# Optimization experiments

Measured on AMD Instinct MI355X. Metric: run time of the kernel, lower is better.

Reference implementation:

```python
import jax, jax.numpy as jnp
import numpy as np

N = 100000   # nodes
E = 3200000  # edges (avg degree 32)
D0, D1, D2, OUT = 128, 64, 64, 10


def setup_inputs() -> dict:
    key = jax.random.key(0)
    ks = jax.random.split(key, 6)
    x = jax.random.normal(ks[0], (N, D0), jnp.float32)
    edge_index = jax.random.randint(ks[1], (2, E), 0, N, jnp.int32)
    Wa1 = jax.random.normal(ks[2], (D0, D1), jnp.float32) / np.sqrt(D0).astype(np.float32)
    ba1 = jnp.zeros((D1,), jnp.float32)
    Wa2 = jax.random.normal(ks[3], (D1, D2), jnp.float32) / np.sqrt(D1).astype(np.float32)
    ba2 = jnp.zeros((D2,), jnp.float32)
    Wl = jax.random.normal(ks[4], (D2 * D2, OUT), jnp.float32) / np.sqrt(D2 * D2).astype(np.float32)
    bl = jnp.zeros((OUT,), jnp.float32)
    return {"x": x, "edge_index": edge_index, "Wa1": Wa1, "ba1": ba1,
            "Wa2": Wa2, "ba2": ba2, "Wl": Wl, "bl": bl}


def _gcn(x, W, b, src, dst, norm):
    # GCNConv: D^{-1/2} (A+I) D^{-1/2} X W + b  (self-loops already in src/dst)
    h = x @ W                                  # [N, Dout]
    m = h[src] * norm[:, None]                 # gather + scale  [E+N, Dout]
    return jax.ops.segment_sum(m, dst, num_segments=N) + b


def reference(x, edge_index, Wa1, ba1, Wa2, ba2, Wl, bl):
    loops = jnp.arange(N, dtype=edge_index.dtype)
    src = jnp.concatenate([edge_index[0], loops])
    dst = jnp.concatenate([edge_index[1], loops])
    deg = jax.ops.segment_sum(jnp.ones_like(src, jnp.float32), dst, num_segments=N)
    dinv = jax.lax.rsqrt(deg)                  # deg >= 1 thanks to self-loops
    norm = dinv[src] * dinv[dst]

    a1 = _gcn(x, Wa1, ba1, src, dst, norm)
    a2 = _gcn(a1, Wa2, ba2, src, dst, norm)
    # Original reuses gcn_a1/gcn_a2 for the x-path, so x_2 == a_2 exactly.
    x2 = a2
    h = a2.T @ x2                              # [D2, D2] attention-style readout
    o = h.reshape(1, -1) @ Wl + bl             # [1, OUT]
    return jax.nn.softmax(o, axis=-1)
```

## Files before the change

kernel.cpp:

```cpp
#include <hip/hip_runtime.h>


#define CHUNK 4096
#define BSH   8

__global__ __launch_bounds__(256) void hist_pass(const int* __restrict__ dst,
                                                 int* __restrict__ ghist,
                                                 int E, int nblk, int nbuck) {
    __shared__ int lcnt[512];
    const int blk = blockIdx.x;
    for (int i = threadIdx.x; i < nbuck; i += 256) lcnt[i] = 0;
    __syncthreads();
    const int base = blk * CHUNK;
    const int end  = min(base + CHUNK, E);
    for (int e = base + threadIdx.x; e < end; e += 256) {
        int d = __builtin_nontemporal_load(&dst[e]);
        atomicAdd(&lcnt[d >> BSH], 1);
    }
    __syncthreads();
    for (int b = threadIdx.x; b < nbuck; b += 256)
        ghist[(size_t)b * nblk + blk] = lcnt[b];
}

__global__ __launch_bounds__(256) void scan_blocks(int* __restrict__ ghist,
                                                   int* __restrict__ btot, int nblk) {
    __shared__ int sh[256];
    int* g = ghist + (size_t)blockIdx.x * nblk;
    const int tid = threadIdx.x;
    int carry = 0;
    for (int base = 0; base < nblk; base += 256) {
        int i = base + tid;
        int v = (i < nblk) ? g[i] : 0;
        sh[tid] = v;
        __syncthreads();
        for (int off = 1; off < 256; off <<= 1) {
            int t = (tid >= off) ? sh[tid - off] : 0;
            __syncthreads();
            sh[tid] += t;
            __syncthreads();
        }
        if (i < nblk) g[i] = carry + sh[tid] - v;
        int tot = sh[255];
        __syncthreads();
        carry += tot;
    }
    if (tid == 0) btot[blockIdx.x] = carry;
}

__global__ void scan_bstart(const int* __restrict__ btot, int* __restrict__ bstart, int nb) {
    __shared__ int sh[512];
    const int tid = threadIdx.x;
    int v = (tid < nb) ? btot[tid] : 0;
    sh[tid] = v;
    __syncthreads();
    for (int off = 1; off < 512; off <<= 1) {
        int t = (tid >= off) ? sh[tid - off] : 0;
        __syncthreads();
        sh[tid] += t;
        __syncthreads();
    }
    if (tid < nb) bstart[tid] = sh[tid] - v;
}

__global__ __launch_bounds__(256) void place_pass(const int* __restrict__ src,
                                                  const int* __restrict__ dst,
                                                  const int* __restrict__ ghist,
                                                  const int* __restrict__ bstart,
                                                  uint2* __restrict__ bedges,
                                                  int E, int nblk, int nbuck) {
    __shared__ int off[512];
    const int blk = blockIdx.x;
    for (int b = threadIdx.x; b < nbuck; b += 256)
        off[b] = bstart[b] + ghist[(size_t)b * nblk + blk];
    __syncthreads();
    const int base = blk * CHUNK;
    const int end  = min(base + CHUNK, E);
    for (int e = base + threadIdx.x; e < end; e += 256) {
        int d = __builtin_nontemporal_load(&dst[e]);
        int s = __builtin_nontemporal_load(&src[e]);
        int pos = atomicAdd(&off[d >> BSH], 1);
        bedges[pos] = make_uint2((unsigned)s, (unsigned)(d & 255));
    }
}

__global__ __launch_bounds__(256) void bucket_csr(const uint2* __restrict__ bedges,
                                                  const int* __restrict__ btot,
                                                  const int* __restrict__ bstart,
                                                  float* __restrict__ dinv,
                                                  int* __restrict__ rowptr,
                                                  int* __restrict__ rowend,
                                                  int* __restrict__ ssorted, int N) {
    __shared__ int lcnt[256];
    __shared__ int sc[256];
    __shared__ int lcur[256];
    const int b   = blockIdx.x;
    const int tid = threadIdx.x;
    const int cnt  = btot[b];
    const int base = bstart[b];
    lcnt[tid] = 0;
    __syncthreads();
    for (int i = tid; i < cnt; i += 256)
        atomicAdd(&lcnt[(int)bedges[base + i].y], 1);
    __syncthreads();
    int c = lcnt[tid];
    sc[tid] = c;
    __syncthreads();
    for (int off = 1; off < 256; off <<= 1) {
        int t = (tid >= off) ? sc[tid - off] : 0;
        __syncthreads();
        sc[tid] += t;
        __syncthreads();
    }
    const int excl = sc[tid] - c;
    const int n = (b << BSH) + tid;
    if (n < N) {
        dinv[n]   = rsqrtf((float)c + 1.0f);
        rowptr[n] = base + excl;
        rowend[n] = base + excl + c;
    }
    lcur[tid] = excl;
    __syncthreads();
    for (int i = tid; i < cnt; i += 256) {
        uint2 e = bedges[base + i];
        int pos = atomicAdd(&lcur[(int)e.y], 1);
        ssorted[base + pos] = (int)e.x;
    }
}

template <int K>
__global__ __launch_bounds__(256) void gemm_tiled(const float* __restrict__ A,
                                                  const float* __restrict__ W,
                                                  const float* __restrict__ dinv,
                                                  float* __restrict__ H, int N) {
    constexpr int KC = 32;
    __shared__ float xs[64][KC + 4];
    __shared__ float ws[KC][64];
    const int tid  = threadIdx.x;
    const int tx   = tid & 15;
    const int ty   = tid >> 4;
    const int base = blockIdx.x * 64;

    float acc[4][4] = {{0.f}};

    for (int kc = 0; kc < K; kc += KC) {
        for (int idx = tid; idx < 512; idx += 256) {
            int node = idx >> 3, k4 = idx & 7;
            int n = base + node;
            float4 v = make_float4(0.f, 0.f, 0.f, 0.f);
            if (n < N) v = *(const float4*)&A[(long long)n * K + kc + k4 * 4];
            *(float4*)&xs[node][k4 * 4] = v;
        }
        for (int idx = tid; idx < 512; idx += 256) {
            int k = idx >> 4, c4 = idx & 15;
            *(float4*)&ws[k][c4 * 4] = *(const float4*)&W[(long long)(kc + k) * 64 + c4 * 4];
        }
        __syncthreads();

#pragma unroll
        for (int k = 0; k < KC; k += 4) {
            float4 xv[4], wv[4];
#pragma unroll
            for (int i = 0; i < 4; ++i) xv[i] = *(const float4*)&xs[ty * 4 + i][k];
#pragma unroll
            for (int j = 0; j < 4; ++j) wv[j] = *(const float4*)&ws[k + j][tx * 4];
#pragma unroll
            for (int i = 0; i < 4; ++i) {
                float xi[4] = {xv[i].x, xv[i].y, xv[i].z, xv[i].w};
#pragma unroll
                for (int j = 0; j < 4; ++j) {
                    acc[i][0] += xi[j] * wv[j].x;
                    acc[i][1] += xi[j] * wv[j].y;
                    acc[i][2] += xi[j] * wv[j].z;
                    acc[i][3] += xi[j] * wv[j].w;
                }
            }
        }
        __syncthreads();
    }

#pragma unroll
    for (int i = 0; i < 4; ++i) {
        int n = base + ty * 4 + i;
        if (n < N) {
            float d = dinv[n];
            float4 r = make_float4(d * acc[i][0], d * acc[i][1], d * acc[i][2], d * acc[i][3]);
            *(float4*)&H[(long long)n * 64 + tx * 4] = r;
        }
    }
}

__global__ void agg_csr(const int* __restrict__ rowptr, const int* __restrict__ endptr,
                        const int* __restrict__ ssorted, const float* __restrict__ dinv,
                        const float* __restrict__ H, const float* __restrict__ bias,
                        float* __restrict__ out, int N) {
    const int wid  = (int)(((long long)blockIdx.x * blockDim.x + threadIdx.x) >> 6);
    if (wid >= N) return;
    const int lane = threadIdx.x & 63;
    const int g    = lane >> 4;
    const int fl   = lane & 15;
    const float4* __restrict__ Hv = (const float4*)H;

    const int   n   = wid;
    const int   beg = rowptr[n];
    const int   end = endptr[n];

    float4 acc = make_float4(0.f, 0.f, 0.f, 0.f);
    for (int e = beg + g; e < end; e += 4) {
        int    s  = ssorted[e];
        float4 hv = Hv[(long long)s * 16 + fl];
        acc.x += hv.x; acc.y += hv.y; acc.z += hv.z; acc.w += hv.w;
    }
    acc.x += __shfl_xor(acc.x, 16); acc.y += __shfl_xor(acc.y, 16);
    acc.z += __shfl_xor(acc.z, 16); acc.w += __shfl_xor(acc.w, 16);
    acc.x += __shfl_xor(acc.x, 32); acc.y += __shfl_xor(acc.y, 32);
    acc.z += __shfl_xor(acc.z, 32); acc.w += __shfl_xor(acc.w, 32);

    if (g == 0) {
        float4 selfv = Hv[(long long)n * 16 + fl];
        float4 bv    = ((const float4*)bias)[fl];
        float  dn    = dinv[n];
        float4 res;
        res.x = bv.x + dn * (selfv.x + acc.x);
        res.y = bv.y + dn * (selfv.y + acc.y);
        res.z = bv.z + dn * (selfv.z + acc.z);
        res.w = bv.w + dn * (selfv.w + acc.w);
        ((float4*)out)[(long long)n * 16 + fl] = res;
    }
}

__global__ void outer_reduce(const float* __restrict__ A2, float* __restrict__ h64, int N) {
    __shared__ float rows[8][64];
    const int tid = threadIdx.x;
    const int col = tid & 63;
    const int rg  = tid >> 6;
    float acc[16];
#pragma unroll
    for (int i = 0; i < 16; ++i) acc[i] = 0.f;

    int npb   = (N + gridDim.x - 1) / gridDim.x;
    int start = blockIdx.x * npb;
    int end   = min(start + npb, N);
    for (int nb = start; nb < end; nb += 8) {
        int cnt = min(8, end - nb);
        __syncthreads();
        for (int idx = tid; idx < cnt * 64; idx += 256)
            rows[idx >> 6][idx & 63] = A2[(long long)(nb + (idx >> 6)) * 64 + (idx & 63)];
        __syncthreads();
        for (int r = 0; r < cnt; ++r) {
            float vc = rows[r][col];
#pragma unroll
            for (int i = 0; i < 16; ++i)
                acc[i] += rows[r][rg * 16 + i] * vc;
        }
    }
#pragma unroll
    for (int i = 0; i < 16; ++i)
        atomicAdd(&h64[(rg * 16 + i) * 64 + col], acc[i]);
}

__global__ void final_kernel(const float* __restrict__ h64, const float* __restrict__ Wl,
                             const float* __restrict__ bl, float* __restrict__ out) {
    __shared__ float red[256];
    __shared__ float o[10];
    const int tid = threadIdx.x;
    float acc[10];
#pragma unroll
    for (int k = 0; k < 10; ++k) acc[k] = 0.f;
    for (int i = tid; i < 4096; i += 256) {
        float v = h64[i];
#pragma unroll
        for (int k = 0; k < 10; ++k) acc[k] += v * Wl[i * 10 + k];
    }
    for (int k = 0; k < 10; ++k) {
        red[tid] = acc[k];
        __syncthreads();
        for (int s = 128; s > 0; s >>= 1) {
            if (tid < s) red[tid] += red[tid + s];
            __syncthreads();
        }
        if (tid == 0) o[k] = red[0] + bl[k];
        __syncthreads();
    }
    if (tid == 0) {
        float m = o[0];
        for (int k = 1; k < 10; ++k) m = fmaxf(m, o[k]);
        float s = 0.f, e[10];
        for (int k = 0; k < 10; ++k) { e[k] = expf(o[k] - m); s += e[k]; }
        for (int k = 0; k < 10; ++k) out[k] = e[k] / s;
    }
}

extern "C" void kernel_launch(void* const* d_in, const int* in_sizes, int n_in,
                              void* d_out, int out_size, void* d_ws, size_t ws_size,
                              hipStream_t stream) {
    const float* x   = (const float*)d_in[0];
    const int*   ei  = (const int*)d_in[1];
    const float* Wa1 = (const float*)d_in[2];
    const float* ba1 = (const float*)d_in[3];
    const float* Wa2 = (const float*)d_in[4];
    const float* ba2 = (const float*)d_in[5];
    const float* Wl  = (const float*)d_in[6];
    const float* bl  = (const float*)d_in[7];
    float* out = (float*)d_out;

    const int N = in_sizes[0] / 128;
    const int E = in_sizes[1] / 2;
    const int* src = ei;
    const int* dst = ei + E;

    const int nblk  = (E + CHUNK - 1) / CHUNK;
    const int nbuck = (N + 255) >> BSH;

    char* wsb = (char*)d_ws;
    float* bufH   = (float*)wsb;
    float* bufA   = bufH + (size_t)N * 64;
    uint2* bedges = (uint2*)wsb;
    int*   ghist  = (int*)(wsb + (size_t)E * 8);
    int*   btot   = ghist + (size_t)nbuck * nblk;
    int*   bstart = btot + 512;
    char*  tail   = wsb + (size_t)N * 128 * 4;
    float* dinv   = (float*)tail;               tail += (size_t)N * 4;
    float* h64    = (float*)tail;               tail += 4096 * 4;
    int*   rowptr = (int*)tail;                 tail += (size_t)N * 4;
    int*   rowend = (int*)tail;                 tail += (size_t)N * 4;
    int*   ssorted= (int*)tail;                 tail += (size_t)E * 4;

    hist_pass<<<nblk, 256, 0, stream>>>(dst, ghist, E, nblk, nbuck);
    scan_blocks<<<nbuck, 256, 0, stream>>>(ghist, btot, nblk);
    scan_bstart<<<1, 512, 0, stream>>>(btot, bstart, nbuck);
    place_pass<<<nblk, 256, 0, stream>>>(src, dst, ghist, bstart, bedges, E, nblk, nbuck);
    bucket_csr<<<nbuck, 256, 0, stream>>>(bedges, btot, bstart, dinv, rowptr, rowend, ssorted, N);

    gemm_tiled<128><<<(N + 63) / 64, 256, 0, stream>>>(x, Wa1, dinv, bufH, N);
    agg_csr<<<(N + 3) / 4, 256, 0, stream>>>(rowptr, rowend, ssorted, dinv, bufH, ba1, bufA, N);

    gemm_tiled<64><<<(N + 63) / 64, 256, 0, stream>>>(bufA, Wa2, dinv, bufH, N);
    agg_csr<<<(N + 3) / 4, 256, 0, stream>>>(rowptr, rowend, ssorted, dinv, bufH, ba2, bufA, N);

    hipMemsetAsync(h64, 0, 4096 * sizeof(float), stream);
    outer_reduce<<<512, 256, 0, stream>>>(bufA, h64, N);
    final_kernel<<<1, 256, 0, stream>>>(h64, Wl, bl, out);
}
```

Baseline: 547.9 us.

## Store hidden features feature-planar and aggregate in sixteen cache-sized passes

The GEMM now writes H as 16 planes of float4, one per group of four features, instead of node-major rows. Aggregation runs one pass per plane, with one wavefront per node gathering a single float4 per edge, so each pass gathers from a table of about 1.6 MB that should stay in L2. The cost is that the sorted-source list is read 16 times, and with an average degree near 32 about half the lanes in each wavefront sit idle. The outer-product reduction now writes per-block partials followed by a reduction kernel instead of using atomics, and the final kernel gives each output one wavefront with a shuffle reduction.

```diff
diff --git a/kernel.cpp b/kernel.cpp
--- a/kernel.cpp
+++ b/kernel.cpp
@@ -127,7 +127,7 @@
     }
 }
 
-template <int K>
+template <int K, bool PM_IN>
 __global__ __launch_bounds__(256) void gemm_tiled(const float* __restrict__ A,
                                                   const float* __restrict__ W,
                                                   const float* __restrict__ dinv,
@@ -139,16 +139,28 @@
     const int tx   = tid & 15;
     const int ty   = tid >> 4;
     const int base = blockIdx.x * 64;
+    const float4* __restrict__ Av4 = (const float4*)A;
+    float4* __restrict__ Hp4 = (float4*)H;
 
     float acc[4][4] = {{0.f}};
 
     for (int kc = 0; kc < K; kc += KC) {
-        for (int idx = tid; idx < 512; idx += 256) {
-            int node = idx >> 3, k4 = idx & 7;
-            int n = base + node;
-            float4 v = make_float4(0.f, 0.f, 0.f, 0.f);
-            if (n < N) v = *(const float4*)&A[(long long)n * K + kc + k4 * 4];
-            *(float4*)&xs[node][k4 * 4] = v;
+        if (PM_IN) {
+            for (int idx = tid; idx < 512; idx += 256) {
+                int node = idx & 63, k4l = idx >> 6;
+                int n = base + node;
+                float4 v = make_float4(0.f, 0.f, 0.f, 0.f);
+                if (n < N) v = Av4[(size_t)(kc / 4 + k4l) * N + n];
+                *(float4*)&xs[node][k4l * 4] = v;
+            }
+        } else {
+            for (int idx = tid; idx < 512; idx += 256) {
+                int node = idx >> 3, k4 = idx & 7;
+                int n = base + node;
+                float4 v = make_float4(0.f, 0.f, 0.f, 0.f);
+                if (n < N) v = *(const float4*)&A[(long long)n * K + kc + k4 * 4];
+                *(float4*)&xs[node][k4 * 4] = v;
+            }
         }
         for (int idx = tid; idx < 512; idx += 256) {
             int k = idx >> 4, c4 = idx & 15;
@@ -184,55 +196,61 @@
         if (n < N) {
             float d = dinv[n];
             float4 r = make_float4(d * acc[i][0], d * acc[i][1], d * acc[i][2], d * acc[i][3]);
-            *(float4*)&H[(long long)n * 64 + tx * 4] = r;
-        }
-    }
-}
-
-__global__ void agg_csr(const int* __restrict__ rowptr, const int* __restrict__ endptr,
-                        const int* __restrict__ ssorted, const float* __restrict__ dinv,
-                        const float* __restrict__ H, const float* __restrict__ bias,
-                        float* __restrict__ out, int N) {
-    const int wid  = (int)(((long long)blockIdx.x * blockDim.x + threadIdx.x) >> 6);
-    if (wid >= N) return;
+            Hp4[(size_t)tx * N + n] = r;
+        }
+    }
+}
+
+#define NPASS 16
+__global__ __launch_bounds__(256) void agg_pass(const int* __restrict__ rowptr,
+                                                const int* __restrict__ rowend,
+                                                const int* __restrict__ ssorted,
+                                                const float* __restrict__ dinv,
+                                                const float* __restrict__ H,
+                                                const float* __restrict__ bias,
+                                                float* __restrict__ out,
+                                                int N, int npb) {
+    const int pass = blockIdx.x / npb;
+    const int nb   = blockIdx.x % npb;
+    const int n    = nb * 4 + (threadIdx.x >> 6);
+    if (n >= N) return;
     const int lane = threadIdx.x & 63;
-    const int g    = lane >> 4;
-    const int fl   = lane & 15;
-    const float4* __restrict__ Hv = (const float4*)H;
-
-    const int   n   = wid;
-    const int   beg = rowptr[n];
-    const int   end = endptr[n];
-
-    float4 acc = make_float4(0.f, 0.f, 0.f, 0.f);
-    for (int e = beg + g; e < end; e += 4) {
-        int    s  = ssorted[e];
-        float4 hv = Hv[(long long)s * 16 + fl];
-        acc.x += hv.x; acc.y += hv.y; acc.z += hv.z; acc.w += hv.w;
-    }
-    acc.x += __shfl_xor(acc.x, 16); acc.y += __shfl_xor(acc.y, 16);
-    acc.z += __shfl_xor(acc.z, 16); acc.w += __shfl_xor(acc.w, 16);
-    acc.x += __shfl_xor(acc.x, 32); acc.y += __shfl_xor(acc.y, 32);
-    acc.z += __shfl_xor(acc.z, 32); acc.w += __shfl_xor(acc.w, 32);
-
-    if (g == 0) {
-        float4 selfv = Hv[(long long)n * 16 + fl];
-        float4 bv    = ((const float4*)bias)[fl];
-        float  dn    = dinv[n];
-        float4 res;
-        res.x = bv.x + dn * (selfv.x + acc.x);
-        res.y = bv.y + dn * (selfv.y + acc.y);
-        res.z = bv.z + dn * (selfv.z + acc.z);
-        res.w = bv.w + dn * (selfv.w + acc.w);
-        ((float4*)out)[(long long)n * 16 + fl] = res;
-    }
-}
-
-__global__ void outer_reduce(const float* __restrict__ A2, float* __restrict__ h64, int N) {
+    const float4* __restrict__ Hs = (const float4*)H + (size_t)pass * N;
+
+    const int beg = rowptr[n];
+    const int end = rowend[n];
+
+    float4 a = make_float4(0.f, 0.f, 0.f, 0.f);
+    for (int e = beg + lane; e < end; e += 64) {
+        int    s = __builtin_nontemporal_load(&ssorted[e]);
+        float4 h = Hs[s];
+        a.x += h.x; a.y += h.y; a.z += h.z; a.w += h.w;
+    }
+#pragma unroll
+    for (int m = 1; m < 64; m <<= 1) {
+        a.x += __shfl_xor(a.x, m); a.y += __shfl_xor(a.y, m);
+        a.z += __shfl_xor(a.z, m); a.w += __shfl_xor(a.w, m);
+    }
+    if (lane == 0) {
+        float  dn = dinv[n];
+        float4 sv = Hs[n];
+        float4 bv = ((const float4*)bias)[pass];
+        float4 r;
+        r.x = bv.x + dn * (sv.x + a.x);
+        r.y = bv.y + dn * (sv.y + a.y);
+        r.z = bv.z + dn * (sv.z + a.z);
+        r.w = bv.w + dn * (sv.w + a.w);
+        ((float4*)out)[(size_t)pass * N + n] = r;
+    }
+}
+
+__global__ __launch_bounds__(256) void outer_partial(const float* __restrict__ A2,
+                                                     float* __restrict__ partial, int N) {
     __shared__ float rows[8][64];
     const int tid = threadIdx.x;
     const int col = tid & 63;
     const int rg  = tid >> 6;
+    const float4* __restrict__ Av4 = (const float4*)A2;
     float acc[16];
 #pragma unroll
     for (int i = 0; i < 16; ++i) acc[i] = 0.f;
@@ -243,8 +261,13 @@
     for (int nb = start; nb < end; nb += 8) {
         int cnt = min(8, end - nb);
         __syncthreads();
-        for (int idx = tid; idx < cnt * 64; idx += 256)
-            rows[idx >> 6][idx & 63] = A2[(long long)(nb + (idx >> 6)) * 64 + (idx & 63)];
+        for (int idx = tid; idx < 128; idx += 256) {
+            int node = idx & 7, c4 = idx >> 3;
+            if (node < cnt) {
+                float4 v = Av4[(size_t)c4 * N + (nb + node)];
+                *(float4*)&rows[node][c4 * 4] = v;
+            }
+        }
         __syncthreads();
         for (int r = 0; r < cnt; ++r) {
             float vc = rows[r][col];
@@ -253,39 +276,35 @@
                 acc[i] += rows[r][rg * 16 + i] * vc;
         }
     }
+    float* p = partial + (size_t)blockIdx.x * 4096;
 #pragma unroll
     for (int i = 0; i < 16; ++i)
-        atomicAdd(&h64[(rg * 16 + i) * 64 + col], acc[i]);
+        p[(rg * 16 + i) * 64 + col] = acc[i];
+}
+
+__global__ void outer_final(const float* __restrict__ partial, float* __restrict__ h64, int nblk) {
+    int idx = blockIdx.x * blockDim.x + threadIdx.x;
+    float s = 0.f;
+    for (int b = 0; b < nblk; ++b) s += partial[(size_t)b * 4096 + idx];
+    h64[idx] = s;
 }
 
 __global__ void final_kernel(const float* __restrict__ h64, const float* __restrict__ Wl,
                              const float* __restrict__ bl, float* __restrict__ out) {
-    __shared__ float red[256];
     __shared__ float o[10];
-    const int tid = threadIdx.x;
-    float acc[10];
-#pragma unroll
-    for (int k = 0; k < 10; ++k) acc[k] = 0.f;
-    for (int i = tid; i < 4096; i += 256) {
-        float v = h64[i];
-#pragma unroll
-        for (int k = 0; k < 10; ++k) acc[k] += v * Wl[i * 10 + k];
-    }
-    for (int k = 0; k < 10; ++k) {
-        red[tid] = acc[k];
-        __syncthreads();
-        for (int s = 128; s > 0; s >>= 1) {
-            if (tid < s) red[tid] += red[tid + s];
-            __syncthreads();
-        }
-        if (tid == 0) o[k] = red[0] + bl[k];
-        __syncthreads();
-    }
-    if (tid == 0) {
-        float m = o[0];
-        for (int k = 1; k < 10; ++k) m = fmaxf(m, o[k]);
+    const int w    = threadIdx.x >> 6;
+    const int lane = threadIdx.x & 63;
+    float acc = 0.f;
+    for (int i = lane; i < 4096; i += 64) acc += h64[i] * Wl[i * 10 + w];
+#pragma unroll
+    for (int m = 1; m < 64; m <<= 1) acc += __shfl_xor(acc, m);
+    if (lane == 0) o[w] = acc + bl[w];
+    __syncthreads();
+    if (threadIdx.x == 0) {
+        float mx = o[0];
+        for (int k = 1; k < 10; ++k) mx = fmaxf(mx, o[k]);
         float s = 0.f, e[10];
-        for (int k = 0; k < 10; ++k) { e[k] = expf(o[k] - m); s += e[k]; }
+        for (int k = 0; k < 10; ++k) { e[k] = expf(o[k] - mx); s += e[k]; }
         for (int k = 0; k < 10; ++k) out[k] = e[k] / s;
     }
 }
@@ -310,10 +329,12 @@
 
     const int nblk  = (E + CHUNK - 1) / CHUNK;
     const int nbuck = (N + 255) >> BSH;
+    const int npb   = (N + 3) / 4;
 
     char* wsb = (char*)d_ws;
     float* bufH   = (float*)wsb;
     float* bufA   = bufH + (size_t)N * 64;
+    float* partial= bufH;
     uint2* bedges = (uint2*)wsb;
     int*   ghist  = (int*)(wsb + (size_t)E * 8);
     int*   btot   = ghist + (size_t)nbuck * nblk;
@@ -331,13 +352,13 @@
     place_pass<<<nblk, 256, 0, stream>>>(src, dst, ghist, bstart, bedges, E, nblk, nbuck);
     bucket_csr<<<nbuck, 256, 0, stream>>>(bedges, btot, bstart, dinv, rowptr, rowend, ssorted, N);
 
-    gemm_tiled<128><<<(N + 63) / 64, 256, 0, stream>>>(x, Wa1, dinv, bufH, N);
-    agg_csr<<<(N + 3) / 4, 256, 0, stream>>>(rowptr, rowend, ssorted, dinv, bufH, ba1, bufA, N);
-
-    gemm_tiled<64><<<(N + 63) / 64, 256, 0, stream>>>(bufA, Wa2, dinv, bufH, N);
-    agg_csr<<<(N + 3) / 4, 256, 0, stream>>>(rowptr, rowend, ssorted, dinv, bufH, ba2, bufA, N);
-
-    hipMemsetAsync(h64, 0, 4096 * sizeof(float), stream);
-    outer_reduce<<<512, 256, 0, stream>>>(bufA, h64, N);
-    final_kernel<<<1, 256, 0, stream>>>(h64, Wl, bl, out);
-}
+    gemm_tiled<128, false><<<(N + 63) / 64, 256, 0, stream>>>(x, Wa1, dinv, bufH, N);
+    agg_pass<<<NPASS * npb, 256, 0, stream>>>(rowptr, rowend, ssorted, dinv, bufH, ba1, bufA, N, npb);
+
+    gemm_tiled<64, true><<<(N + 63) / 64, 256, 0, stream>>>(bufA, Wa2, dinv, bufH, N);
+    agg_pass<<<NPASS * npb, 256, 0, stream>>>(rowptr, rowend, ssorted, dinv, bufH, ba2, bufA, N, npb);
+
+    outer_partial<<<512, 256, 0, stream>>>(bufA, partial, N);
+    outer_final<<<16, 256, 0, stream>>>(partial, h64, 512);
+    final_kernel<<<1, 640, 0, stream>>>(h64, Wl, bl, out);
+}
```

Result: slower. 1.420 ms (+159.2%).

## Store GEMM outputs as bf16 and pack bucketed edges into 32-bit words

Applied to the files above, without the earlier changes.

The GEMM epilogue now writes the scaled features as packed bf16 pairs, and the aggregation kernel gathers and unpacks these, halving bytes per random neighbor gather. Edge bucketing packs source id and low destination bits into one 32-bit word, halving the intermediate edge buffer traffic. The cost is reduced feature precision in the aggregation inputs and an assumption that node ids fit in 24 bits.

```diff
diff --git a/kernel.cpp b/kernel.cpp
--- a/kernel.cpp
+++ b/kernel.cpp
@@ -3,6 +3,15 @@
 
 #define CHUNK 4096
 #define BSH   8
+
+__device__ __forceinline__ unsigned short f2bf(float f) {
+    unsigned u = __float_as_uint(f);
+    unsigned r = (u + 0x7FFFu + ((u >> 16) & 1u)) >> 16;
+    return (unsigned short)r;
+}
+__device__ __forceinline__ float bf2f(unsigned h) {
+    return __uint_as_float(h << 16);
+}
 
 __global__ __launch_bounds__(256) void hist_pass(const int* __restrict__ dst,
                                                  int* __restrict__ ghist,
@@ -66,7 +75,7 @@
                                                   const int* __restrict__ dst,
                                                   const int* __restrict__ ghist,
                                                   const int* __restrict__ bstart,
-                                                  uint2* __restrict__ bedges,
+                                                  unsigned* __restrict__ bedges,
                                                   int E, int nblk, int nbuck) {
     __shared__ int off[512];
     const int blk = blockIdx.x;
@@ -79,11 +88,11 @@
         int d = __builtin_nontemporal_load(&dst[e]);
         int s = __builtin_nontemporal_load(&src[e]);
         int pos = atomicAdd(&off[d >> BSH], 1);
-        bedges[pos] = make_uint2((unsigned)s, (unsigned)(d & 255));
-    }
-}
-
-__global__ __launch_bounds__(256) void bucket_csr(const uint2* __restrict__ bedges,
+        bedges[pos] = ((unsigned)s << 8) | (unsigned)(d & 255);
+    }
+}
+
+__global__ __launch_bounds__(256) void bucket_csr(const unsigned* __restrict__ bedges,
                                                   const int* __restrict__ btot,
                                                   const int* __restrict__ bstart,
                                                   float* __restrict__ dinv,
@@ -100,7 +109,7 @@
     lcnt[tid] = 0;
     __syncthreads();
     for (int i = tid; i < cnt; i += 256)
-        atomicAdd(&lcnt[(int)bedges[base + i].y], 1);
+        atomicAdd(&lcnt[(int)(bedges[base + i] & 255u)], 1);
     __syncthreads();
     int c = lcnt[tid];
     sc[tid] = c;
@@ -121,9 +130,9 @@
     lcur[tid] = excl;
     __syncthreads();
     for (int i = tid; i < cnt; i += 256) {
-        uint2 e = bedges[base + i];
-        int pos = atomicAdd(&lcur[(int)e.y], 1);
-        ssorted[base + pos] = (int)e.x;
+        unsigned e = bedges[base + i];
+        int pos = atomicAdd(&lcur[(int)(e & 255u)], 1);
+        ssorted[base + pos] = (int)(e >> 8);
     }
 }
 
@@ -131,7 +140,7 @@
 __global__ __launch_bounds__(256) void gemm_tiled(const float* __restrict__ A,
                                                   const float* __restrict__ W,
                                                   const float* __restrict__ dinv,
-                                                  float* __restrict__ H, int N) {
+                                                  uint2* __restrict__ Hb, int N) {
     constexpr int KC = 32;
     __shared__ float xs[64][KC + 4];
     __shared__ float ws[KC][64];
@@ -183,32 +192,36 @@
         int n = base + ty * 4 + i;
         if (n < N) {
             float d = dinv[n];
-            float4 r = make_float4(d * acc[i][0], d * acc[i][1], d * acc[i][2], d * acc[i][3]);
-            *(float4*)&H[(long long)n * 64 + tx * 4] = r;
+            uint2 o;
+            o.x = (unsigned)f2bf(d * acc[i][0]) | ((unsigned)f2bf(d * acc[i][1]) << 16);
+            o.y = (unsigned)f2bf(d * acc[i][2]) | ((unsigned)f2bf(d * acc[i][3]) << 16);
+            Hb[(size_t)n * 16 + tx] = o;
         }
     }
 }
 
 __global__ void agg_csr(const int* __restrict__ rowptr, const int* __restrict__ endptr,
                         const int* __restrict__ ssorted, const float* __restrict__ dinv,
-                        const float* __restrict__ H, const float* __restrict__ bias,
+                        const uint2* __restrict__ Hb, const float* __restrict__ bias,
                         float* __restrict__ out, int N) {
     const int wid  = (int)(((long long)blockIdx.x * blockDim.x + threadIdx.x) >> 6);
     if (wid >= N) return;
     const int lane = threadIdx.x & 63;
     const int g    = lane >> 4;
     const int fl   = lane & 15;
-    const float4* __restrict__ Hv = (const float4*)H;
-
-    const int   n   = wid;
-    const int   beg = rowptr[n];
-    const int   end = endptr[n];
+
+    const int n   = wid;
+    const int beg = rowptr[n];
+    const int end = endptr[n];
 
     float4 acc = make_float4(0.f, 0.f, 0.f, 0.f);
     for (int e = beg + g; e < end; e += 4) {
-        int    s  = ssorted[e];
-        float4 hv = Hv[(long long)s * 16 + fl];
-        acc.x += hv.x; acc.y += hv.y; acc.z += hv.z; acc.w += hv.w;
+        int   s = __builtin_nontemporal_load(&ssorted[e]);
+        uint2 c = Hb[(size_t)s * 16 + fl];
+        acc.x += bf2f(c.x & 0xFFFFu);
+        acc.y += bf2f(c.x >> 16);
+        acc.z += bf2f(c.y & 0xFFFFu);
+        acc.w += bf2f(c.y >> 16);
     }
     acc.x += __shfl_xor(acc.x, 16); acc.y += __shfl_xor(acc.y, 16);
     acc.z += __shfl_xor(acc.z, 16); acc.w += __shfl_xor(acc.w, 16);
@@ -216,15 +229,15 @@
     acc.z += __shfl_xor(acc.z, 32); acc.w += __shfl_xor(acc.w, 32);
 
     if (g == 0) {
-        float4 selfv = Hv[(long long)n * 16 + fl];
-        float4 bv    = ((const float4*)bias)[fl];
-        float  dn    = dinv[n];
+        uint2  sc = Hb[(size_t)n * 16 + fl];
+        float4 bv = ((const float4*)bias)[fl];
+        float  dn = dinv[n];
         float4 res;
-        res.x = bv.x + dn * (selfv.x + acc.x);
-        res.y = bv.y + dn * (selfv.y + acc.y);
-        res.z = bv.z + dn * (selfv.z + acc.z);
-        res.w = bv.w + dn * (selfv.w + acc.w);
-        ((float4*)out)[(long long)n * 16 + fl] = res;
+        res.x = bv.x + dn * (bf2f(sc.x & 0xFFFFu) + acc.x);
+        res.y = bv.y + dn * (bf2f(sc.x >> 16)     + acc.y);
+        res.z = bv.z + dn * (bf2f(sc.y & 0xFFFFu) + acc.z);
+        res.w = bv.w + dn * (bf2f(sc.y >> 16)     + acc.w);
+        ((float4*)out)[(size_t)n * 16 + fl] = res;
     }
 }
 
@@ -312,13 +325,13 @@
     const int nbuck = (N + 255) >> BSH;
 
     char* wsb = (char*)d_ws;
-    float* bufH   = (float*)wsb;
-    float* bufA   = bufH + (size_t)N * 64;
-    uint2* bedges = (uint2*)wsb;
-    int*   ghist  = (int*)(wsb + (size_t)E * 8);
+    uint2* Hb     = (uint2*)wsb;
+    float* bufA   = (float*)(wsb + (size_t)N * 128);
+    unsigned* bedges = (unsigned*)wsb;
+    int*   ghist  = (int*)(wsb + (size_t)E * 4);
     int*   btot   = ghist + (size_t)nbuck * nblk;
     int*   bstart = btot + 512;
-    char*  tail   = wsb + (size_t)N * 128 * 4;
+    char*  tail   = wsb + (size_t)N * 128 + (size_t)N * 256;
     float* dinv   = (float*)tail;               tail += (size_t)N * 4;
     float* h64    = (float*)tail;               tail += 4096 * 4;
     int*   rowptr = (int*)tail;                 tail += (size_t)N * 4;
@@ -331,11 +344,11 @@
     place_pass<<<nblk, 256, 0, stream>>>(src, dst, ghist, bstart, bedges, E, nblk, nbuck);
     bucket_csr<<<nbuck, 256, 0, stream>>>(bedges, btot, bstart, dinv, rowptr, rowend, ssorted, N);
 
-    gemm_tiled<128><<<(N + 63) / 64, 256, 0, stream>>>(x, Wa1, dinv, bufH, N);
-    agg_csr<<<(N + 3) / 4, 256, 0, stream>>>(rowptr, rowend, ssorted, dinv, bufH, ba1, bufA, N);
-
-    gemm_tiled<64><<<(N + 63) / 64, 256, 0, stream>>>(bufA, Wa2, dinv, bufH, N);
-    agg_csr<<<(N + 3) / 4, 256, 0, stream>>>(rowptr, rowend, ssorted, dinv, bufH, ba2, bufA, N);
+    gemm_tiled<128><<<(N + 63) / 64, 256, 0, stream>>>(x, Wa1, dinv, Hb, N);
+    agg_csr<<<(N + 3) / 4, 256, 0, stream>>>(rowptr, rowend, ssorted, dinv, Hb, ba1, bufA, N);
+
+    gemm_tiled<64><<<(N + 63) / 64, 256, 0, stream>>>(bufA, Wa2, dinv, Hb, N);
+    agg_csr<<<(N + 3) / 4, 256, 0, stream>>>(rowptr, rowend, ssorted, dinv, Hb, ba2, bufA, N);
 
     hipMemsetAsync(h64, 0, 4096 * sizeof(float), stream);
     outer_reduce<<<512, 256, 0, stream>>>(bufA, h64, N);
```

Measured after the change: 551.3 us. About the same (+0.6%).
